# Optimization experiments

Hardware: AMD Instinct MI355X
Metric: run time of the kernel (lower is better)

## Reference

```python
import jax, jax.numpy as jnp
import numpy as np

NUM_Q = 4
CODEBOOK = 1024
DIM = 256
COMMIT = 0.25


def setup_inputs() -> dict:
    key = jax.random.key(0)
    k1, k2 = jax.random.split(key)
    x = jax.random.normal(k1, (16, 8192, DIM), dtype=jnp.float32)
    embeddings = jax.random.normal(k2, (NUM_Q, CODEBOOK, DIM), dtype=jnp.float32)
    return {"x": x, "embeddings": embeddings}


def _vq_layer(residual, emb):
    # residual: (..., D), emb: (K, D)
    shp = residual.shape
    flat = residual.reshape(-1, DIM)  # (N, D)
    # squared euclidean distances (N, K)
    d = (jnp.sum(flat * flat, axis=1, keepdims=True)
         + jnp.sum(emb * emb, axis=1)
         - 2.0 * flat @ emb.T)
    idx = jnp.argmin(d, axis=1)               # (N,)
    q = emb[idx].reshape(shp)                  # gather == one-hot matmul
    e_latent = jnp.mean((jax.lax.stop_gradient(q) - residual) ** 2)
    q_latent = jnp.mean((q - jax.lax.stop_gradient(residual)) ** 2)
    commitment = COMMIT * e_latent
    # straight-through estimator
    q_st = residual + jax.lax.stop_gradient(q - residual)
    return q_st, idx.reshape(shp[:-1]), q_latent + commitment, commitment, q_latent


def reference(x, embeddings):
    residual = x
    quantized_out = jnp.zeros_like(x)
    all_idx = []
    vq_loss = jnp.float32(0.0)
    commit_loss = jnp.float32(0.0)
    codebook_loss = jnp.float32(0.0)
    for i in range(NUM_Q):
        q_st, idx, vq_l, c_l, cb_l = _vq_layer(residual, embeddings[i])
        quantized_out = quantized_out + q_st
        residual = residual - q_st
        all_idx.append(idx)
        vq_loss = vq_loss + vq_l
        commit_loss = commit_loss + c_l
        codebook_loss = codebook_loss + cb_l
    indices = jnp.stack(all_idx, axis=0)  # (NUM_Q, B, T)
    return quantized_out, indices, vq_loss, commit_loss, codebook_loss
```

## Files before the change

### kernel.cpp

```cpp
#include <hip/hip_runtime.h>

#define SUMTOPO 2

#define NUM_Q   4
#define KCODE   1024
#define DIM     256
#define NROWS   131072
#define QELEMS  33554432
#define MARGIN  3e-3f

typedef _Float16 f16x8 __attribute__((ext_vector_type(8)));
typedef float    f32x4 __attribute__((ext_vector_type(4)));

__global__ __launch_bounds__(64) void rvq_prep(const float* __restrict__ emb,
                                               _Float16* __restrict__ efrag,
                                               float* __restrict__ e2,
                                               double* __restrict__ loss)
{
    const int bid  = blockIdx.x;
    const int lane = threadIdx.x;
    const int layer = bid >> 6, tile = bid & 63;
    const int c = tile*16 + (lane & 15);
    const int g = lane >> 4;
    const float* ep = emb + ((size_t)layer*KCODE + c)*DIM;

    double s2 = 0.0;
    #pragma unroll
    for (int j = 0; j < 8; ++j) {
        const int k0 = j*32 + 8*g;
        float4 a = *(const float4*)(ep + k0);
        float4 b = *(const float4*)(ep + k0 + 4);
        float v[8] = {a.x,a.y,a.z,a.w,b.x,b.y,b.z,b.w};
        f16x8 hh, ll;
        #pragma unroll
        for (int x = 0; x < 8; ++x) {
            double dv = (double)v[x];
            s2 += dv*dv;
            float m2 = -2.0f*v[x];
            _Float16 h = (_Float16)m2;
            hh[x] = h;
            ll[x] = (_Float16)((m2 - (float)h)*4096.0f);
        }
        size_t base = (((size_t)(bid*8 + j)*2 + 0)*64 + lane)*8;
        *(f16x8*)(efrag + base)       = hh;
        *(f16x8*)(efrag + base + 512) = ll;
    }
    s2 += __shfl_xor(s2, 16);
    s2 += __shfl_xor(s2, 32);
    if (g == 0) e2[layer*KCODE + c] = (float)s2;
    if (bid == 0 && lane < 4) loss[lane] = 0.0;
}

__device__ __forceinline__ float np_pw_base(const float* v, int n) {
    #pragma clang fp contract(off)
    float r[8];
    #pragma unroll
    for (int j = 0; j < 8; ++j) r[j] = v[j];
    int i = 8;
    for (; i < n - (n % 8); i += 8) {
        #pragma unroll
        for (int j = 0; j < 8; ++j) r[j] = r[j] + v[i+j];
    }
    float res = ((r[0] + r[1]) + (r[2] + r[3])) + ((r[4] + r[5]) + (r[6] + r[7]));
    for (; i < n; ++i) res = res + v[i];
    return res;
}

__device__ __forceinline__ float np_simd512_128(const float* p) {
    #pragma clang fp contract(off)
    float s[16], U[4];
    #pragma unroll
    for (int l = 0; l < 16; ++l) {
        s[l] = ((p[l] + p[16+l]) + (p[32+l] + p[48+l]))
             + ((p[64+l] + p[80+l]) + (p[96+l] + p[112+l]));
    }
    #pragma unroll
    for (int i = 0; i < 4; ++i) U[i] = (s[i] + s[i+8]) + (s[i+4] + s[i+12]);
    return (U[0] + U[2]) + (U[1] + U[3]);
}

__device__ __forceinline__ float np_sum256(const float* v) {
    #pragma clang fp contract(off)
#if SUMTOPO == 0
    return np_pw_base(v, 128) + np_pw_base(v + 128, 128);
#elif SUMTOPO == 1
    float right = np_pw_base(v + 121, 64) + np_pw_base(v + 185, 71);
    return v[0] + (np_pw_base(v + 1, 120) + right);
#else
    return np_simd512_128(v) + np_simd512_128(v + 128);
#endif
}

__global__ __launch_bounds__(256, 2) void rvq_layer(
    const float* __restrict__ rin, float* __restrict__ rout,
    const float* __restrict__ emb,
    const _Float16* __restrict__ efrag,
    const float* __restrict__ e2,
    float* __restrict__ idx_out,
    double* __restrict__ loss_slot)
{
    __shared__ __align__(16) _Float16 lt[2][8][2][64][8];
    __shared__ __align__(16) float    e2l[KCODE];
    __shared__ __align__(16) float    s_remu[4][DIM];
    __shared__ double wsum[4];

    const int tid  = threadIdx.x;
    const int w    = tid >> 6;
    const int lane = tid & 63;
    const int col  = lane & 15;
    const int g    = lane >> 4;
    const int r0   = blockIdx.x*128 + w*32;

    {
        f32x4 v = *(const f32x4*)(e2 + tid*4);
        *(f32x4*)(e2l + tid*4) = v;
    }

    f16x8 rh[2][8], rl[2][8];
    #pragma unroll
    for (int t = 0; t < 2; ++t) {
        const float* rp = rin + (size_t)(r0 + 16*t + col)*DIM + 8*g;
        #pragma unroll
        for (int j = 0; j < 8; ++j) {
            float4 a = *(const float4*)(rp + j*32);
            float4 b = *(const float4*)(rp + j*32 + 4);
            float v[8] = {a.x,a.y,a.z,a.w,b.x,b.y,b.z,b.w};
            #pragma unroll
            for (int x = 0; x < 8; ++x) {
                _Float16 h = (_Float16)v[x];
                rh[t][j][x] = h;
                rl[t][j][x] = (_Float16)((v[x] - (float)h)*4096.0f);
            }
        }
    }

    const uint4* gsrc = (const uint4*)efrag;
    {
        uint4 s0 = gsrc[tid], s1 = gsrc[256+tid], s2 = gsrc[512+tid], s3 = gsrc[768+tid];
        uint4* lw = (uint4*)&lt[0][0][0][0][0];
        lw[tid] = s0; lw[256+tid] = s1; lw[512+tid] = s2; lw[768+tid] = s3;
    }
    __syncthreads();

    float m1[2]  = {3.4e38f, 3.4e38f};
    float m2v[2] = {3.4e38f, 3.4e38f};
    int   i1[2]  = {0, 0};
    int   i2[2]  = {0, 0};

    for (int ct = 0; ct < 64; ++ct) {
        const int cur = ct & 1;
        uint4 p0, p1, p2, p3;
        if (ct < 63) {
            const uint4* gn = gsrc + (size_t)(ct+1)*1024;
            p0 = gn[tid]; p1 = gn[256+tid]; p2 = gn[512+tid]; p3 = gn[768+tid];
        }
        f32x4 acch[2] = {{0.f,0.f,0.f,0.f},{0.f,0.f,0.f,0.f}};
        f32x4 accl[2] = {{0.f,0.f,0.f,0.f},{0.f,0.f,0.f,0.f}};
        #pragma unroll
        for (int j = 0; j < 8; ++j) {
            f16x8 ah = *(const f16x8*)&lt[cur][j][0][lane][0];
            f16x8 al = *(const f16x8*)&lt[cur][j][1][lane][0];
            acch[0] = __builtin_amdgcn_mfma_f32_16x16x32_f16(ah, rh[0][j], acch[0], 0,0,0);
            acch[1] = __builtin_amdgcn_mfma_f32_16x16x32_f16(ah, rh[1][j], acch[1], 0,0,0);
            accl[0] = __builtin_amdgcn_mfma_f32_16x16x32_f16(al, rh[0][j], accl[0], 0,0,0);
            accl[1] = __builtin_amdgcn_mfma_f32_16x16x32_f16(al, rh[1][j], accl[1], 0,0,0);
            accl[0] = __builtin_amdgcn_mfma_f32_16x16x32_f16(ah, rl[0][j], accl[0], 0,0,0);
            accl[1] = __builtin_amdgcn_mfma_f32_16x16x32_f16(ah, rl[1][j], accl[1], 0,0,0);
        }
        f32x4 e2v = *(const f32x4*)(e2l + ct*16 + 4*g);
        #pragma unroll
        for (int t = 0; t < 2; ++t) {
            #pragma unroll
            for (int r = 0; r < 4; ++r) {
                float s = acch[t][r] + accl[t][r]*(1.0f/4096.0f) + e2v[r];
                int   k = ct*16 + 4*g + r;
                bool c1 = s < m1[t];
                bool c2 = s < m2v[t];
                m2v[t] = c1 ? m1[t] : (c2 ? s : m2v[t]);
                i2[t]  = c1 ? i1[t] : (c2 ? k : i2[t]);
                m1[t]  = c1 ? s : m1[t];
                i1[t]  = c1 ? k : i1[t];
            }
        }
        __syncthreads();
        if (ct < 63) {
            uint4* lw = (uint4*)&lt[cur^1][0][0][0][0];
            lw[tid] = p0; lw[256+tid] = p1; lw[512+tid] = p2; lw[768+tid] = p3;
        }
        __syncthreads();
    }

    #pragma unroll
    for (int t = 0; t < 2; ++t) {
        #pragma unroll
        for (int off = 16; off < 64; off <<= 1) {
            float om1 = __shfl_xor(m1[t], off), om2 = __shfl_xor(m2v[t], off);
            int   oi1 = __shfl_xor(i1[t], off), oi2 = __shfl_xor(i2[t], off);
            bool aL = (m1[t] < om1) || (m1[t] == om1 && i1[t] < oi1);
            float M1 = aL ? m1[t] : om1;  int I1 = aL ? i1[t] : oi1;
            float cv = aL ? om1 : m1[t];  int ci = aL ? oi1 : i1[t];
            float sv = aL ? m2v[t] : om2; int si = aL ? i2[t] : oi2;
            bool bL = (cv < sv) || (cv == sv && ci < si);
            m2v[t] = bL ? cv : sv; i2[t] = bL ? ci : si;
            m1[t] = M1; i1[t] = I1;
        }
    }

    #pragma unroll
    for (int t = 0; t < 2; ++t) {
        bool flag = (m2v[t] - m1[t]) < MARGIN;
        unsigned long long mask = __ballot(flag) & 0xFFFFull;
        while (mask) {
            int lnp = __ffsll((unsigned long long)mask) - 1; mask &= mask - 1;
            int row = r0 + 16*t + lnp;
            int ca = __shfl(i1[t], lnp);
            int cb = __shfl(i2[t], lnp);
            float4 rv = *(const float4*)(rin + (size_t)row*DIM + 4*lane);
            *(float4*)&s_remu[w][4*lane] = rv;
            asm volatile("s_waitcnt lgkmcnt(0)" ::: "memory");
            float d;
            {
                #pragma clang fp contract(off)
                const int   cand = (lane == 0) ? ca : cb;
                const float* ep  = emb + (size_t)cand*DIM;
                const float* rp  = &s_remu[w][0];
                float m = 0.f;
                for (int k = 0; k < DIM; ++k) m = __builtin_fmaf(rp[k], ep[k], m);
                float tmp[DIM];
                for (int k = 0; k < DIM; ++k) tmp[k] = ep[k]*ep[k];
                float se = np_sum256(tmp);
                for (int k = 0; k < DIM; ++k) tmp[k] = rp[k]*rp[k];
                float sr = np_sum256(tmp);
                d = (sr + se) - 2.0f*m;
            }
            float da = __shfl(d, 0), db = __shfl(d, 1);
            int wnr = (db < da) ? cb : ((da < db) ? ca : (ca < cb ? ca : cb));
            if (col == lnp) i1[t] = wnr;
        }
    }

    if (lane < 32) {
        int v = (lane < 16) ? i1[0] : i1[1];
        idx_out[r0 + lane] = (float)v;
    }

    double lacc = 0.0;
    #pragma unroll 4
    for (int i = 0; i < 32; ++i) {
        #pragma clang fp contract(off)
        int kr = __shfl((i < 16) ? i1[0] : i1[1], i & 15);
        int row = r0 + i;
        float4 rv = *(const float4*)(rin + (size_t)row*DIM + 4*lane);
        float4 ev = *(const float4*)(emb + (size_t)kr*DIM + 4*lane);
        float t0 = ev.x - rv.x, t1g = ev.y - rv.y, t2g = ev.z - rv.z, t3g = ev.w - rv.w;
        float q0 = rv.x + t0,  q1 = rv.y + t1g,  q2 = rv.z + t2g,  q3 = rv.w + t3g;
        float4 nv;
        nv.x = rv.x - q0; nv.y = rv.y - q1; nv.z = rv.z - q2; nv.w = rv.w - q3;
        *(float4*)(rout + (size_t)row*DIM + 4*lane) = nv;
        lacc += (double)(t0*t0) + (double)(t1g*t1g) + (double)(t2g*t2g) + (double)(t3g*t3g);
    }
    #pragma unroll
    for (int o = 32; o; o >>= 1) lacc += __shfl_xor(lacc, o);
    if (lane == 0) wsum[w] = lacc;
    __syncthreads();
    if (tid == 0) atomicAdd(loss_slot, wsum[0]+wsum[1]+wsum[2]+wsum[3]);
}

__global__ void rvq_final(const float* __restrict__ x, float* __restrict__ outq,
                          const double* __restrict__ loss, float* __restrict__ lossout)
{
    size_t i = (size_t)blockIdx.x*blockDim.x + threadIdx.x;
    size_t stride = (size_t)gridDim.x*blockDim.x;
    const float4* x4 = (const float4*)x;
    float4* o4 = (float4*)outq;
    for (size_t e = i; e < (size_t)QELEMS/4; e += stride) {
        float4 xv = x4[e];
        float4 rv = o4[e];
        float4 o; o.x = xv.x - rv.x; o.y = xv.y - rv.y; o.z = xv.z - rv.z; o.w = xv.w - rv.w;
        o4[e] = o;
    }
    if (blockIdx.x == 0 && threadIdx.x == 0) {
        double tot = (loss[0]+loss[1]+loss[2]+loss[3]) * (1.0/(double)QELEMS);
        lossout[0] = (float)(1.25*tot);
        lossout[1] = (float)(0.25*tot);
        lossout[2] = (float)tot;
    }
}

extern "C" void kernel_launch(void* const* d_in, const int* in_sizes, int n_in,
                              void* d_out, int out_size, void* d_ws, size_t ws_size,
                              hipStream_t stream)
{
    (void)in_sizes; (void)n_in; (void)out_size; (void)ws_size;
    const float* x   = (const float*)d_in[0];
    const float* emb = (const float*)d_in[1];
    float* out      = (float*)d_out;
    float* rbuf     = out;
    float* idx_base = out + QELEMS;
    float* loss_out = out + QELEMS + (size_t)NUM_Q*NROWS;

    _Float16* efrag = (_Float16*)d_ws;
    float*    e2    = (float*)((char*)d_ws + 4u*1024u*1024u);
    double*   loss  = (double*)((char*)d_ws + 4u*1024u*1024u + 16384u);

    rvq_prep<<<NUM_Q*64, 64, 0, stream>>>(emb, efrag, e2, loss);
    for (int q = 0; q < NUM_Q; ++q) {
        const float* rin = (q == 0) ? x : rbuf;
        rvq_layer<<<NROWS/128, 256, 0, stream>>>(
            rin, rbuf,
            emb   + (size_t)q*KCODE*DIM,
            efrag + (size_t)q*64*8192,
            e2    + (size_t)q*KCODE,
            idx_base + (size_t)q*NROWS,
            loss + q);
    }
    rvq_final<<<2048, 256, 0, stream>>>(x, rbuf, loss, loss_out);
}
```

Measured before the change: 993.8 us.

## Use single-fp16 MFMA distances with top-4 packed keys and exact fp32 rescoring

Drops the hi/lo fp16 split of embeddings and residuals, so the distance GEMM runs one MFMA pass instead of three. Candidate tracking becomes a top-4 list of packed uint keys (truncated distance bits plus code index), with e2 offset by 256 so the float bits sort as unsigned. Any candidate within a wider margin of the best is rescored exactly in fp32. It also doubles rows per wave to reuse each codebook LDS tile more, prefetches tiles straight into LDS with global_load_lds, drops one barrier per tile, and folds the final x-minus-residual pass into the last layer launch. The cost is that correctness now depends on the margin heuristic catching every fp16 error, and more rows may need the slow rescoring path.

```diff
diff --git a/kernel.cpp b/kernel.cpp
--- a/kernel.cpp
+++ b/kernel.cpp
@@ -1,26 +1,35 @@
 #include <hip/hip_runtime.h>
 
-#define SUMTOPO 2
 
 #define NUM_Q   4
 #define KCODE   1024
 #define DIM     256
 #define NROWS   131072
 #define QELEMS  33554432
-#define MARGIN  3e-3f
+#define MARGIN_FLAG 0.40f
+#define KMASK   0xFFFFFC00u
 
 typedef _Float16 f16x8 __attribute__((ext_vector_type(8)));
 typedef float    f32x4 __attribute__((ext_vector_type(4)));
 
+__device__ __forceinline__ void gload_lds16(const void* g, void* l) {
+    __builtin_amdgcn_global_load_lds(
+        (const __attribute__((address_space(1))) void*)g,
+        (__attribute__((address_space(3))) void*)l, 16, 0, 0);
+}
+__device__ __forceinline__ float dqk(unsigned k) { return __uint_as_float(k & KMASK); }
+__device__ __forceinline__ unsigned umin2(unsigned a, unsigned b) { return a < b ? a : b; }
+__device__ __forceinline__ unsigned umax2(unsigned a, unsigned b) { return a > b ? a : b; }
+
 __global__ __launch_bounds__(64) void rvq_prep(const float* __restrict__ emb,
                                                _Float16* __restrict__ efrag,
-                                               float* __restrict__ e2,
+                                               float* __restrict__ e2b,
                                                double* __restrict__ loss)
 {
     const int bid  = blockIdx.x;
     const int lane = threadIdx.x;
-    const int layer = bid >> 6, tile = bid & 63;
-    const int c = tile*16 + (lane & 15);
+    const int layer = bid >> 6;
+    const int c = (bid & 63)*16 + (lane & 15);
     const int g = lane >> 4;
     const float* ep = emb + ((size_t)layer*KCODE + c)*DIM;
 
@@ -31,75 +40,53 @@
         float4 a = *(const float4*)(ep + k0);
         float4 b = *(const float4*)(ep + k0 + 4);
         float v[8] = {a.x,a.y,a.z,a.w,b.x,b.y,b.z,b.w};
-        f16x8 hh, ll;
+        f16x8 hh;
         #pragma unroll
         for (int x = 0; x < 8; ++x) {
             double dv = (double)v[x];
             s2 += dv*dv;
-            float m2 = -2.0f*v[x];
-            _Float16 h = (_Float16)m2;
-            hh[x] = h;
-            ll[x] = (_Float16)((m2 - (float)h)*4096.0f);
-        }
-        size_t base = (((size_t)(bid*8 + j)*2 + 0)*64 + lane)*8;
-        *(f16x8*)(efrag + base)       = hh;
-        *(f16x8*)(efrag + base + 512) = ll;
+            hh[x] = (_Float16)(-2.0f*v[x]);
+        }
+        *(f16x8*)(efrag + ((size_t)(bid*8 + j)*64 + lane)*8) = hh;
     }
     s2 += __shfl_xor(s2, 16);
     s2 += __shfl_xor(s2, 32);
-    if (g == 0) e2[layer*KCODE + c] = (float)s2;
+    if (g == 0) e2b[layer*KCODE + c] = (float)(s2 + 256.0);
     if (bid == 0 && lane < 4) loss[lane] = 0.0;
 }
 
-__device__ __forceinline__ float np_pw_base(const float* v, int n) {
-    #pragma clang fp contract(off)
-    float r[8];
-    #pragma unroll
-    for (int j = 0; j < 8; ++j) r[j] = v[j];
-    int i = 8;
-    for (; i < n - (n % 8); i += 8) {
-        #pragma unroll
-        for (int j = 0; j < 8; ++j) r[j] = r[j] + v[i+j];
-    }
-    float res = ((r[0] + r[1]) + (r[2] + r[3])) + ((r[4] + r[5]) + (r[6] + r[7]));
-    for (; i < n; ++i) res = res + v[i];
-    return res;
-}
-
-__device__ __forceinline__ float np_simd512_128(const float* p) {
+__device__ __forceinline__ float np_sq128(const float* p) {
     #pragma clang fp contract(off)
     float s[16], U[4];
     #pragma unroll
     for (int l = 0; l < 16; ++l) {
-        s[l] = ((p[l] + p[16+l]) + (p[32+l] + p[48+l]))
-             + ((p[64+l] + p[80+l]) + (p[96+l] + p[112+l]));
+        s[l] = ((p[l]*p[l] + p[16+l]*p[16+l]) + (p[32+l]*p[32+l] + p[48+l]*p[48+l]))
+             + ((p[64+l]*p[64+l] + p[80+l]*p[80+l]) + (p[96+l]*p[96+l] + p[112+l]*p[112+l]));
     }
     #pragma unroll
     for (int i = 0; i < 4; ++i) U[i] = (s[i] + s[i+8]) + (s[i+4] + s[i+12]);
     return (U[0] + U[2]) + (U[1] + U[3]);
 }
-
-__device__ __forceinline__ float np_sum256(const float* v) {
+__device__ __noinline__ float np_dist(const float* rp, const float* ep) {
     #pragma clang fp contract(off)
-#if SUMTOPO == 0
-    return np_pw_base(v, 128) + np_pw_base(v + 128, 128);
-#elif SUMTOPO == 1
-    float right = np_pw_base(v + 121, 64) + np_pw_base(v + 185, 71);
-    return v[0] + (np_pw_base(v + 1, 120) + right);
-#else
-    return np_simd512_128(v) + np_simd512_128(v + 128);
-#endif
+    float m = 0.f;
+    #pragma unroll 1
+    for (int k = 0; k < DIM; ++k) m = __builtin_fmaf(rp[k], ep[k], m);
+    float se = np_sq128(ep) + np_sq128(ep + 128);
+    float sr = np_sq128(rp) + np_sq128(rp + 128);
+    return (sr + se) - 2.0f*m;
 }
 
 __global__ __launch_bounds__(256, 2) void rvq_layer(
     const float* __restrict__ rin, float* __restrict__ rout,
     const float* __restrict__ emb,
     const _Float16* __restrict__ efrag,
-    const float* __restrict__ e2,
+    const float* __restrict__ e2b,
     float* __restrict__ idx_out,
-    double* __restrict__ loss_slot)
-{
-    __shared__ __align__(16) _Float16 lt[2][8][2][64][8];
+    double* __restrict__ loss_slot,
+    const float* __restrict__ xin)
+{
+    __shared__ __align__(16) _Float16 lt[2][8][64][8];
     __shared__ __align__(16) float    e2l[KCODE];
     __shared__ __align__(16) float    s_remu[4][DIM];
     __shared__ double wsum[4];
@@ -109,16 +96,13 @@
     const int lane = tid & 63;
     const int col  = lane & 15;
     const int g    = lane >> 4;
-    const int r0   = blockIdx.x*128 + w*32;
-
-    {
-        f32x4 v = *(const f32x4*)(e2 + tid*4);
-        *(f32x4*)(e2l + tid*4) = v;
-    }
-
-    f16x8 rh[2][8], rl[2][8];
-    #pragma unroll
-    for (int t = 0; t < 2; ++t) {
+    const int r0   = (blockIdx.x*4 + w)*64;
+
+    *(f32x4*)(e2l + tid*4) = *(const f32x4*)(e2b + tid*4);
+
+    f16x8 rh[4][8];
+    #pragma unroll
+    for (int t = 0; t < 4; ++t) {
         const float* rp = rin + (size_t)(r0 + 16*t + col)*DIM + 8*g;
         #pragma unroll
         for (int j = 0; j < 8; ++j) {
@@ -126,138 +110,131 @@
             float4 b = *(const float4*)(rp + j*32 + 4);
             float v[8] = {a.x,a.y,a.z,a.w,b.x,b.y,b.z,b.w};
             #pragma unroll
-            for (int x = 0; x < 8; ++x) {
-                _Float16 h = (_Float16)v[x];
-                rh[t][j][x] = h;
-                rl[t][j][x] = (_Float16)((v[x] - (float)h)*4096.0f);
-            }
+            for (int x = 0; x < 8; ++x) rh[t][j][x] = (_Float16)v[x];
         }
     }
 
     const uint4* gsrc = (const uint4*)efrag;
-    {
-        uint4 s0 = gsrc[tid], s1 = gsrc[256+tid], s2 = gsrc[512+tid], s3 = gsrc[768+tid];
-        uint4* lw = (uint4*)&lt[0][0][0][0][0];
-        lw[tid] = s0; lw[256+tid] = s1; lw[512+tid] = s2; lw[768+tid] = s3;
-    }
+    char* lbase = (char*)&lt[0][0][0][0];
+    gload_lds16(gsrc + tid,       lbase + tid*16);
+    gload_lds16(gsrc + 256 + tid, lbase + 4096 + tid*16);
+
+    unsigned k1[4], k2[4], k3[4], k4[4];
+    #pragma unroll
+    for (int t = 0; t < 4; ++t) { k1[t]=k2[t]=k3[t]=k4[t]=0xFFFFFFFFu; }
+    const unsigned kor = (unsigned)(g << 2);
+
     __syncthreads();
-
-    float m1[2]  = {3.4e38f, 3.4e38f};
-    float m2v[2] = {3.4e38f, 3.4e38f};
-    int   i1[2]  = {0, 0};
-    int   i2[2]  = {0, 0};
 
     for (int ct = 0; ct < 64; ++ct) {
         const int cur = ct & 1;
-        uint4 p0, p1, p2, p3;
         if (ct < 63) {
-            const uint4* gn = gsrc + (size_t)(ct+1)*1024;
-            p0 = gn[tid]; p1 = gn[256+tid]; p2 = gn[512+tid]; p3 = gn[768+tid];
-        }
-        f32x4 acch[2] = {{0.f,0.f,0.f,0.f},{0.f,0.f,0.f,0.f}};
-        f32x4 accl[2] = {{0.f,0.f,0.f,0.f},{0.f,0.f,0.f,0.f}};
+            char* nb = (char*)&lt[cur^1][0][0][0];
+            gload_lds16(gsrc + (ct+1)*512 + tid,       nb + tid*16);
+            gload_lds16(gsrc + (ct+1)*512 + 256 + tid, nb + 4096 + tid*16);
+        }
+        f32x4 e2v = *(const f32x4*)(e2l + ct*16 + 4*g);
+        f32x4 acc[4] = {e2v, e2v, e2v, e2v};
         #pragma unroll
         for (int j = 0; j < 8; ++j) {
-            f16x8 ah = *(const f16x8*)&lt[cur][j][0][lane][0];
-            f16x8 al = *(const f16x8*)&lt[cur][j][1][lane][0];
-            acch[0] = __builtin_amdgcn_mfma_f32_16x16x32_f16(ah, rh[0][j], acch[0], 0,0,0);
-            acch[1] = __builtin_amdgcn_mfma_f32_16x16x32_f16(ah, rh[1][j], acch[1], 0,0,0);
-            accl[0] = __builtin_amdgcn_mfma_f32_16x16x32_f16(al, rh[0][j], accl[0], 0,0,0);
-            accl[1] = __builtin_amdgcn_mfma_f32_16x16x32_f16(al, rh[1][j], accl[1], 0,0,0);
-            accl[0] = __builtin_amdgcn_mfma_f32_16x16x32_f16(ah, rl[0][j], accl[0], 0,0,0);
-            accl[1] = __builtin_amdgcn_mfma_f32_16x16x32_f16(ah, rl[1][j], accl[1], 0,0,0);
-        }
-        f32x4 e2v = *(const f32x4*)(e2l + ct*16 + 4*g);
-        #pragma unroll
-        for (int t = 0; t < 2; ++t) {
+            f16x8 ah = *(const f16x8*)&lt[cur][j][lane][0];
+            #pragma unroll
+            for (int t = 0; t < 4; ++t)
+                acc[t] = __builtin_amdgcn_mfma_f32_16x16x32_f16(ah, rh[t][j], acc[t], 0,0,0);
+        }
+        const unsigned ctb = (unsigned)(ct << 4);
+        #pragma unroll
+        for (int t = 0; t < 4; ++t) {
             #pragma unroll
             for (int r = 0; r < 4; ++r) {
-                float s = acch[t][r] + accl[t][r]*(1.0f/4096.0f) + e2v[r];
-                int   k = ct*16 + 4*g + r;
-                bool c1 = s < m1[t];
-                bool c2 = s < m2v[t];
-                m2v[t] = c1 ? m1[t] : (c2 ? s : m2v[t]);
-                i2[t]  = c1 ? i1[t] : (c2 ? k : i2[t]);
-                m1[t]  = c1 ? s : m1[t];
-                i1[t]  = c1 ? k : i1[t];
+                unsigned u   = __float_as_uint(acc[t][r]);
+                unsigned key = (u & KMASK) | kor | (ctb + (unsigned)r);
+                unsigned a1 = umin2(k1[t], key), b1 = umax2(k1[t], key); k1[t] = a1;
+                unsigned a2 = umin2(k2[t], b1),  b2 = umax2(k2[t], b1);  k2[t] = a2;
+                unsigned a3 = umin2(k3[t], b2),  b3 = umax2(k3[t], b2);  k3[t] = a3;
+                k4[t] = umin2(k4[t], b3);
             }
         }
         __syncthreads();
-        if (ct < 63) {
-            uint4* lw = (uint4*)&lt[cur^1][0][0][0][0];
-            lw[tid] = p0; lw[256+tid] = p1; lw[512+tid] = p2; lw[768+tid] = p3;
-        }
-        __syncthreads();
-    }
-
-    #pragma unroll
-    for (int t = 0; t < 2; ++t) {
-        #pragma unroll
-        for (int off = 16; off < 64; off <<= 1) {
-            float om1 = __shfl_xor(m1[t], off), om2 = __shfl_xor(m2v[t], off);
-            int   oi1 = __shfl_xor(i1[t], off), oi2 = __shfl_xor(i2[t], off);
-            bool aL = (m1[t] < om1) || (m1[t] == om1 && i1[t] < oi1);
-            float M1 = aL ? m1[t] : om1;  int I1 = aL ? i1[t] : oi1;
-            float cv = aL ? om1 : m1[t];  int ci = aL ? oi1 : i1[t];
-            float sv = aL ? m2v[t] : om2; int si = aL ? i2[t] : oi2;
-            bool bL = (cv < sv) || (cv == sv && ci < si);
-            m2v[t] = bL ? cv : sv; i2[t] = bL ? ci : si;
-            m1[t] = M1; i1[t] = I1;
-        }
-    }
-
-    #pragma unroll
-    for (int t = 0; t < 2; ++t) {
-        bool flag = (m2v[t] - m1[t]) < MARGIN;
-        unsigned long long mask = __ballot(flag) & 0xFFFFull;
-        while (mask) {
-            int lnp = __ffsll((unsigned long long)mask) - 1; mask &= mask - 1;
-            int row = r0 + 16*t + lnp;
-            int ca = __shfl(i1[t], lnp);
-            int cb = __shfl(i2[t], lnp);
+    }
+
+    int   fidx[4];
+    float thrv[4];
+    unsigned rowm[4];
+    #pragma unroll
+    for (int t = 0; t < 4; ++t) {
+        unsigned gm = k1[t];
+        gm = umin2(gm, __shfl_xor(gm, 16));
+        gm = umin2(gm, __shfl_xor(gm, 32));
+        float thr = dqk(gm) + MARGIN_FLAG;
+        bool c1 = (k1[t] != gm) && (dqk(k1[t]) < thr);
+        bool c2 = dqk(k2[t]) < thr;
+        bool c3 = dqk(k3[t]) < thr;
+        bool c4 = dqk(k4[t]) < thr;
+        unsigned long long b = __ballot(c1 || c2 || c3 || c4);
+        rowm[t] = (unsigned)((b | (b>>16) | (b>>32) | (b>>48)) & 0xFFFFull);
+        fidx[t] = (int)(gm & 1023u);
+        thrv[t] = thr;
+    }
+
+    #pragma unroll
+    for (int t = 0; t < 4; ++t) {
+        unsigned m = rowm[t];
+        while (m) {
+            int p = __ffs(m) - 1; m &= m - 1;
+            int row = r0 + 16*t + p;
             float4 rv = *(const float4*)(rin + (size_t)row*DIM + 4*lane);
             *(float4*)&s_remu[w][4*lane] = rv;
             asm volatile("s_waitcnt lgkmcnt(0)" ::: "memory");
-            float d;
-            {
-                #pragma clang fp contract(off)
-                const int   cand = (lane == 0) ? ca : cb;
-                const float* ep  = emb + (size_t)cand*DIM;
-                const float* rp  = &s_remu[w][0];
-                float m = 0.f;
-                for (int k = 0; k < DIM; ++k) m = __builtin_fmaf(rp[k], ep[k], m);
-                float tmp[DIM];
-                for (int k = 0; k < DIM; ++k) tmp[k] = ep[k]*ep[k];
-                float se = np_sum256(tmp);
-                for (int k = 0; k < DIM; ++k) tmp[k] = rp[k]*rp[k];
-                float sr = np_sum256(tmp);
-                d = (sr + se) - 2.0f*m;
-            }
-            float da = __shfl(d, 0), db = __shfl(d, 1);
-            int wnr = (db < da) ? cb : ((da < db) ? ca : (ca < cb ? ca : cb));
-            if (col == lnp) i1[t] = wnr;
-        }
-    }
-
-    if (lane < 32) {
-        int v = (lane < 16) ? i1[0] : i1[1];
-        idx_out[r0 + lane] = (float)v;
-    }
-
+            int srcl = ((lane & 12) << 2) | p;
+            unsigned s1 = __shfl(k1[t], srcl), s2 = __shfl(k2[t], srcl);
+            unsigned s3 = __shfl(k3[t], srcl), s4 = __shfl(k4[t], srcl);
+            int slot = lane & 3;
+            unsigned ksel = slot == 0 ? s1 : (slot == 1 ? s2 : (slot == 2 ? s3 : s4));
+            float thr_p = __shfl(thrv[t], p);
+            bool valid = (lane < 16) && (dqk(ksel) < thr_p);
+            float d = 3.4e38f;
+            int   cc = 0x7FFFFFFF;
+            if (valid) {
+                cc = (int)(ksel & 1023u);
+                d  = np_dist(&s_remu[w][0], emb + (size_t)cc*DIM);
+            }
+            #pragma unroll
+            for (int off = 1; off < 64; off <<= 1) {
+                float od = __shfl_xor(d, off);
+                int   oc = __shfl_xor(cc, off);
+                if (od < d || (od == d && oc < cc)) { d = od; cc = oc; }
+            }
+            if ((lane & 15) == p) fidx[t] = cc;
+        }
+    }
+
+    #pragma unroll
+    for (int t = 0; t < 4; ++t)
+        if (lane < 16) idx_out[r0 + 16*t + lane] = (float)fidx[t];
+
+    const bool last = (xin != nullptr);
     double lacc = 0.0;
-    #pragma unroll 4
-    for (int i = 0; i < 32; ++i) {
-        #pragma clang fp contract(off)
-        int kr = __shfl((i < 16) ? i1[0] : i1[1], i & 15);
-        int row = r0 + i;
-        float4 rv = *(const float4*)(rin + (size_t)row*DIM + 4*lane);
-        float4 ev = *(const float4*)(emb + (size_t)kr*DIM + 4*lane);
-        float t0 = ev.x - rv.x, t1g = ev.y - rv.y, t2g = ev.z - rv.z, t3g = ev.w - rv.w;
-        float q0 = rv.x + t0,  q1 = rv.y + t1g,  q2 = rv.z + t2g,  q3 = rv.w + t3g;
-        float4 nv;
-        nv.x = rv.x - q0; nv.y = rv.y - q1; nv.z = rv.z - q2; nv.w = rv.w - q3;
-        *(float4*)(rout + (size_t)row*DIM + 4*lane) = nv;
-        lacc += (double)(t0*t0) + (double)(t1g*t1g) + (double)(t2g*t2g) + (double)(t3g*t3g);
+    #pragma unroll
+    for (int t = 0; t < 4; ++t) {
+        #pragma unroll 4
+        for (int i = 0; i < 16; ++i) {
+            #pragma clang fp contract(off)
+            int kr = __shfl(fidx[t], i);
+            int row = r0 + 16*t + i;
+            float4 rv = *(const float4*)(rin + (size_t)row*DIM + 4*lane);
+            float4 ev = *(const float4*)(emb + (size_t)kr*DIM + 4*lane);
+            float t0 = ev.x - rv.x, t1 = ev.y - rv.y, t2 = ev.z - rv.z, t3 = ev.w - rv.w;
+            float q0 = rv.x + t0,  q1 = rv.y + t1,  q2 = rv.z + t2,  q3 = rv.w + t3;
+            float4 nv;
+            nv.x = rv.x - q0; nv.y = rv.y - q1; nv.z = rv.z - q2; nv.w = rv.w - q3;
+            if (last) {
+                float4 xv = *(const float4*)(xin + (size_t)row*DIM + 4*lane);
+                nv.x = xv.x - nv.x; nv.y = xv.y - nv.y; nv.z = xv.z - nv.z; nv.w = xv.w - nv.w;
+            }
+            *(float4*)(rout + (size_t)row*DIM + 4*lane) = nv;
+            lacc += (double)(t0*t0) + (double)(t1*t1) + (double)(t2*t2) + (double)(t3*t3);
+        }
     }
     #pragma unroll
     for (int o = 32; o; o >>= 1) lacc += __shfl_xor(lacc, o);
@@ -266,25 +243,12 @@
     if (tid == 0) atomicAdd(loss_slot, wsum[0]+wsum[1]+wsum[2]+wsum[3]);
 }
 
-__global__ void rvq_final(const float* __restrict__ x, float* __restrict__ outq,
-                          const double* __restrict__ loss, float* __restrict__ lossout)
-{
-    size_t i = (size_t)blockIdx.x*blockDim.x + threadIdx.x;
-    size_t stride = (size_t)gridDim.x*blockDim.x;
-    const float4* x4 = (const float4*)x;
-    float4* o4 = (float4*)outq;
-    for (size_t e = i; e < (size_t)QELEMS/4; e += stride) {
-        float4 xv = x4[e];
-        float4 rv = o4[e];
-        float4 o; o.x = xv.x - rv.x; o.y = xv.y - rv.y; o.z = xv.z - rv.z; o.w = xv.w - rv.w;
-        o4[e] = o;
-    }
-    if (blockIdx.x == 0 && threadIdx.x == 0) {
-        double tot = (loss[0]+loss[1]+loss[2]+loss[3]) * (1.0/(double)QELEMS);
-        lossout[0] = (float)(1.25*tot);
-        lossout[1] = (float)(0.25*tot);
-        lossout[2] = (float)tot;
-    }
+__global__ void rvq_loss(const double* __restrict__ loss, float* __restrict__ lossout)
+{
+    double tot = (loss[0]+loss[1]+loss[2]+loss[3]) * (1.0/(double)QELEMS);
+    lossout[0] = (float)(1.25*tot);
+    lossout[1] = (float)(0.25*tot);
+    lossout[2] = (float)tot;
 }
 
 extern "C" void kernel_launch(void* const* d_in, const int* in_sizes, int n_in,
@@ -300,19 +264,19 @@
     float* loss_out = out + QELEMS + (size_t)NUM_Q*NROWS;
 
     _Float16* efrag = (_Float16*)d_ws;
-    float*    e2    = (float*)((char*)d_ws + 4u*1024u*1024u);
-    double*   loss  = (double*)((char*)d_ws + 4u*1024u*1024u + 16384u);
-
-    rvq_prep<<<NUM_Q*64, 64, 0, stream>>>(emb, efrag, e2, loss);
+    float*    e2b   = (float*)((char*)d_ws + 2u*1024u*1024u);
+    double*   loss  = (double*)((char*)d_ws + 2u*1024u*1024u + 16384u);
+
+    rvq_prep<<<NUM_Q*64, 64, 0, stream>>>(emb, efrag, e2b, loss);
     for (int q = 0; q < NUM_Q; ++q) {
-        const float* rin = (q == 0) ? x : rbuf;
-        rvq_layer<<<NROWS/128, 256, 0, stream>>>(
-            rin, rbuf,
+        rvq_layer<<<NROWS/256, 256, 0, stream>>>(
+            (q == 0) ? x : rbuf, rbuf,
             emb   + (size_t)q*KCODE*DIM,
-            efrag + (size_t)q*64*8192,
-            e2    + (size_t)q*KCODE,
+            efrag + (size_t)q*64*4096,
+            e2b   + (size_t)q*KCODE,
             idx_base + (size_t)q*NROWS,
-            loss + q);
-    }
-    rvq_final<<<2048, 256, 0, stream>>>(x, rbuf, loss, loss_out);
-}
+            loss + q,
+            (q == NUM_Q-1) ? x : nullptr);
+    }
+    rvq_loss<<<1, 1, 0, stream>>>(loss, loss_out);
+}
```

After: 1.653 ms. +66.4%, slower.
